# Kernel tuning notes

Hardware: AMD Instinct MI355X
Metric: run time of the kernel (lower is better)

The kernel has to match this reference:

```python
import jax, jax.numpy as jnp
import numpy as np

N, E, DIN, DH, H, B, C = 20000, 320000, 128, 64, 8, 16, 10
NEG_SLOPE = 0.2


def segment_softmax(e, dst, num_nodes):
    # e: [E, H] edge scores, softmax over edges sharing the same dst node
    m = jax.ops.segment_max(e, dst, num_segments=num_nodes)          # [N, H]
    ex = jnp.exp(e - m[dst])                                          # [E, H]
    den = jax.ops.segment_sum(ex, dst, num_segments=num_nodes)       # [N, H]
    return ex / den[dst]


def gat_layer(h, edge_src, edge_dst, W, attn_l, attn_r, bias):
    # h: [N, F_in] -> out: [N, H, DH]  (DGL GATConv math)
    feat = (h @ W).reshape(-1, H, DH)                                 # [N, H, DH]
    el = jnp.einsum('nhd,hd->nh', feat, attn_l)                       # [N, H]
    er = jnp.einsum('nhd,hd->nh', feat, attn_r)                       # [N, H]
    e = jax.nn.leaky_relu(el[edge_src] + er[edge_dst], NEG_SLOPE)     # [E, H]
    alpha = segment_softmax(e, edge_dst, feat.shape[0])               # [E, H]
    msg = feat[edge_src] * alpha[..., None]                           # [E, H, DH]
    out = jax.ops.segment_sum(msg, edge_dst, num_segments=feat.shape[0])
    return out + bias[None, :, :]


def setup_inputs() -> dict:
    key = jax.random.key(0)
    ks = jax.random.split(key, 16)
    s_in = 1.0 / np.sqrt(DIN)
    s_h = 1.0 / np.sqrt(DH)
    return {
        'g_feats': jax.random.normal(ks[0], (N, DIN), jnp.float32),
        'edge_src': jax.random.randint(ks[1], (E,), 0, N),
        'edge_dst': jax.random.randint(ks[2], (E,), 0, N),
        'node_graph_ids': jnp.sort(jax.random.randint(ks[3], (N,), 0, B)),
        'W_in': jax.random.normal(ks[4], (DIN, DH), jnp.float32) * s_in,
        'b_in': jnp.zeros((DH,), jnp.float32),
        'W1': jax.random.normal(ks[5], (DH, H * DH), jnp.float32) * s_h,
        'attn_l1': jax.random.normal(ks[6], (H, DH), jnp.float32) * s_h,
        'attn_r1': jax.random.normal(ks[7], (H, DH), jnp.float32) * s_h,
        'bias1': jnp.zeros((H, DH), jnp.float32),
        'W2': jax.random.normal(ks[8], (DH, H * DH), jnp.float32) * s_h,
        'attn_l2': jax.random.normal(ks[9], (H, DH), jnp.float32) * s_h,
        'attn_r2': jax.random.normal(ks[10], (H, DH), jnp.float32) * s_h,
        'bias2': jnp.zeros((H, DH), jnp.float32),
        'W_head': jax.random.normal(ks[11], (DH, C), jnp.float32) * s_h,
        'b_head': jnp.zeros((C,), jnp.float32),
    }


def reference(g_feats, edge_src, edge_dst, node_graph_ids,
              W_in, b_in, W1, attn_l1, attn_r1, bias1,
              W2, attn_l2, attn_r2, bias2, W_head, b_head):
    h = g_feats @ W_in + b_in                                          # input layer
    h = gat_layer(h, edge_src, edge_dst, W1, attn_l1, attn_r1, bias1)  # [N,H,DH]
    h = jax.nn.relu(h.mean(axis=1))                                    # head-mean + relu
    h = gat_layer(h, edge_src, edge_dst, W2, attn_l2, attn_r2, bias2)
    h = h.mean(axis=1)                                                 # [N, DH]
    # mean readout per graph
    sums = jax.ops.segment_sum(h, node_graph_ids, num_segments=B)      # [B, DH]
    cnt = jax.ops.segment_sum(jnp.ones((h.shape[0],), h.dtype), node_graph_ids, num_segments=B)
    hg = sums / jnp.maximum(cnt, 1.0)[:, None]
    return jax.nn.softmax(hg @ W_head + b_head, axis=-1)               # [B, C]
```

## Files before the change

kernel.cpp:

```cpp
#include <hip/hip_runtime.h>
#include <hip/hip_bf16.h>
#include <math.h>


#define NEG_SLOPE 0.2f

typedef float f32x2 __attribute__((ext_vector_type(2)));

__device__ __forceinline__ float bf2f(__hip_bfloat16 b) { return __bfloat162float(b); }

__device__ __forceinline__ unsigned int pack4_fp8(float a, float b, float c, float d) {
    unsigned int u = 0;
    u = __builtin_amdgcn_cvt_pk_fp8_f32(a, b, u, false);
    u = __builtin_amdgcn_cvt_pk_fp8_f32(c, d, u, true);
    return u;
}
__device__ __forceinline__ void unpack8_fp8(uint2 u, float* f) {
    f32x2 a = __builtin_amdgcn_cvt_pk_f32_fp8(u.x, false);
    f32x2 b = __builtin_amdgcn_cvt_pk_f32_fp8(u.x, true);
    f32x2 c = __builtin_amdgcn_cvt_pk_f32_fp8(u.y, false);
    f32x2 d = __builtin_amdgcn_cvt_pk_f32_fp8(u.y, true);
    f[0] = a[0]; f[1] = a[1]; f[2] = b[0]; f[3] = b[1];
    f[4] = c[0]; f[5] = c[1]; f[6] = d[0]; f[7] = d[1];
}

__global__ void hist_kernel(const int* __restrict__ dst, int* __restrict__ cnt, int E) {
    int e = blockIdx.x * 256 + threadIdx.x;
    if (e < E) atomicAdd(&cnt[dst[e]], 1);
}

__global__ __launch_bounds__(1024) void scan_kernel(const int* __restrict__ cnt,
                                                    int* __restrict__ row_start,
                                                    int* __restrict__ cursor, int N) {
    __shared__ int part[1024];
    int t = threadIdx.x;
    int CH = (N + 1023) >> 10;
    int beg = t * CH;
    int end = beg + CH; if (end > N) end = N;
    if (beg > N) beg = N;
    int local = 0;
    for (int i = beg; i < end; ++i) local += cnt[i];
    part[t] = local;
    __syncthreads();
    for (int off = 1; off < 1024; off <<= 1) {
        int v = (t >= off) ? part[t - off] : 0;
        __syncthreads();
        part[t] += v;
        __syncthreads();
    }
    int run = part[t] - local;
    for (int i = beg; i < end; ++i) {
        row_start[i] = run; cursor[i] = run;
        run += cnt[i];
    }
    if (t == 1023) row_start[N] = run;
}

__global__ void scatter_kernel(const int* __restrict__ src, const int* __restrict__ dst,
                               int* __restrict__ cursor, int* __restrict__ src_sorted, int E) {
    int e = blockIdx.x * 256 + threadIdx.x;
    if (e < E) {
        int p = atomicAdd(&cursor[dst[e]], 1);
        src_sorted[p] = src[e];
    }
}

__global__ __launch_bounds__(256) void in_gemm(const float* __restrict__ g,
                                               const float* __restrict__ W,
                                               const float* __restrict__ b,
                                               float* __restrict__ h0, int N) {
    __shared__ float gt[128][36];
    int t = threadIdx.x;
    int n0 = blockIdx.x * 32;
#pragma unroll
    for (int i = 0; i < 4; ++i) {
        int ch = t + i * 256;
        int r = ch >> 5, k0 = (ch & 31) << 2;
        float4 v = (n0 + r < N) ? *(const float4*)(g + (size_t)(n0 + r) * 128 + k0)
                                : make_float4(0.f, 0.f, 0.f, 0.f);
        gt[k0 + 0][r] = v.x; gt[k0 + 1][r] = v.y; gt[k0 + 2][r] = v.z; gt[k0 + 3][r] = v.w;
    }
    __syncthreads();
    int c = t & 63, rg = t >> 6;
    float acc[8];
#pragma unroll
    for (int j = 0; j < 8; ++j) acc[j] = 0.f;
#pragma unroll 4
    for (int k = 0; k < 128; ++k) {
        float w = W[k * 64 + c];
        const float* hp = &gt[k][rg * 8];
        float4 ha = *(const float4*)hp;
        float4 hb = *(const float4*)(hp + 4);
        acc[0] = fmaf(ha.x, w, acc[0]);
        acc[1] = fmaf(ha.y, w, acc[1]);
        acc[2] = fmaf(ha.z, w, acc[2]);
        acc[3] = fmaf(ha.w, w, acc[3]);
        acc[4] = fmaf(hb.x, w, acc[4]);
        acc[5] = fmaf(hb.y, w, acc[5]);
        acc[6] = fmaf(hb.z, w, acc[6]);
        acc[7] = fmaf(hb.w, w, acc[7]);
    }
    float bb = b[c];
#pragma unroll
    for (int j = 0; j < 8; ++j) {
        int r = rg * 8 + j;
        if (n0 + r < N) h0[(size_t)(n0 + r) * 64 + c] = acc[j] + bb;
    }
}

__global__ __launch_bounds__(512) void feat_gemm(const float* __restrict__ hin,
                                                 const float* __restrict__ W,
                                                 const float* __restrict__ al,
                                                 const float* __restrict__ ar,
                                                 unsigned char* __restrict__ feat8,
                                                 __hip_bfloat16* __restrict__ el,
                                                 __hip_bfloat16* __restrict__ er, int N) {
    __shared__ float ht[64][36];
    int t = threadIdx.x;
    int n0 = blockIdx.x * 32;
    {
        int r = t >> 4, k0 = (t & 15) << 2;
        float4 v = (n0 + r < N) ? *(const float4*)(hin + (size_t)(n0 + r) * 64 + k0)
                                : make_float4(0.f, 0.f, 0.f, 0.f);
        ht[k0 + 0][r] = v.x; ht[k0 + 1][r] = v.y; ht[k0 + 2][r] = v.z; ht[k0 + 3][r] = v.w;
    }
    __syncthreads();
    int ci = t & 127;
    int c0 = ci << 2;
    int rg = t >> 7;
    int r0 = rg << 3;
    float acc[8][4];
#pragma unroll
    for (int r = 0; r < 8; ++r)
#pragma unroll
        for (int j = 0; j < 4; ++j) acc[r][j] = 0.f;
#pragma unroll 4
    for (int k = 0; k < 64; ++k) {
        float4 w = *(const float4*)(W + k * 512 + c0);
        const float* hp = &ht[k][r0];
        float4 ha = *(const float4*)hp;
        float4 hb = *(const float4*)(hp + 4);
        float hr[8] = {ha.x, ha.y, ha.z, ha.w, hb.x, hb.y, hb.z, hb.w};
        float wv[4] = {w.x, w.y, w.z, w.w};
#pragma unroll
        for (int r = 0; r < 8; ++r)
#pragma unroll
            for (int j = 0; j < 4; ++j)
                acc[r][j] = fmaf(hr[r], wv[j], acc[r][j]);
    }
    float4 va = *(const float4*)(al + c0);
    float4 vb = *(const float4*)(ar + c0);
    int head = ci >> 4;
    float elp[8], erp[8];
#pragma unroll
    for (int r = 0; r < 8; ++r) {
        elp[r] = acc[r][0] * va.x + acc[r][1] * va.y + acc[r][2] * va.z + acc[r][3] * va.w;
        erp[r] = acc[r][0] * vb.x + acc[r][1] * vb.y + acc[r][2] * vb.z + acc[r][3] * vb.w;
        if (n0 + r0 + r < N) {
            *(unsigned int*)(feat8 + (size_t)(n0 + r0 + r) * 512 + c0) =
                pack4_fp8(acc[r][0], acc[r][1], acc[r][2], acc[r][3]);
        }
    }
#pragma unroll
    for (int off = 1; off < 16; off <<= 1)
#pragma unroll
        for (int r = 0; r < 8; ++r) {
            elp[r] += __shfl_xor(elp[r], off, 64);
            erp[r] += __shfl_xor(erp[r], off, 64);
        }
    if ((ci & 15) == 0) {
#pragma unroll
        for (int r = 0; r < 8; ++r) {
            if (n0 + r0 + r < N) {
                el[(size_t)(n0 + r0 + r) * 8 + head] = __float2bfloat16(elp[r]);
                er[(size_t)(n0 + r0 + r) * 8 + head] = __float2bfloat16(erp[r]);
            }
        }
    }
}

template <bool RELU>
__global__ __launch_bounds__(256) void gat_aggregate(
    const unsigned char* __restrict__ feat8, const __hip_bfloat16* __restrict__ el,
    const __hip_bfloat16* __restrict__ er, const float* __restrict__ bias,
    const int* __restrict__ row_start, const int* __restrict__ src_sorted,
    float* __restrict__ hout, int N) {
    int lane = threadIdx.x & 63;
    int n = blockIdx.x * 4 + (threadIdx.x >> 6);
    if (n >= N) return;
    int h = lane >> 3;
    float erh = bf2f(er[(size_t)n * 8 + h]);
    int row = row_start[n];
    int deg = row_start[n + 1] - row;
    const unsigned char* featl = feat8 + lane * 8;

    float acc[8];
#pragma unroll
    for (int j = 0; j < 8; ++j) acc[j] = 0.f;
    float den = 0.f;

    for (int base = 0; base < deg; base += 64) {
        int cnt = min(deg - base, 64);
        int sv = (lane < cnt) ? src_sorted[row + base + lane] : 0;
        int nsub = cnt & ~7;
        for (int i0 = 0; i0 < nsub; i0 += 8) {
            int se = __shfl(sv, i0 + (lane & 7), 64);
            float ve = bf2f(el[(size_t)se * 8 + h]) + erh;
            ve = fmaxf(ve, NEG_SLOPE * ve);
            float am = __expf(ve);
            int hb = lane & 0x38;
#pragma unroll
            for (int e = 0; e < 8; ++e) {
                float a = __shfl(am, hb | e, 64);
                int s = __shfl(sv, i0 + e, 64);
                uint2 u = *(const uint2*)(featl + (size_t)s * 512);
                den += a;
                float f[8];
                unpack8_fp8(u, f);
#pragma unroll
                for (int j = 0; j < 8; ++j) acc[j] = fmaf(a, f[j], acc[j]);
            }
        }
        for (int i = nsub; i < cnt; ++i) {
            int s = __shfl(sv, i, 64);
            uint2 u = *(const uint2*)(featl + (size_t)s * 512);
            float v = bf2f(el[(size_t)s * 8 + h]) + erh;
            v = fmaxf(v, NEG_SLOPE * v);
            float a = __expf(v);
            den += a;
            float f[8];
            unpack8_fp8(u, f);
#pragma unroll
            for (int j = 0; j < 8; ++j) acc[j] = fmaf(a, f[j], acc[j]);
        }
    }

    float invd = deg > 0 ? 1.f / den : 0.f;
    const float4* bp = (const float4*)(bias + lane * 8);
    float4 b0 = bp[0], b1 = bp[1];
    float o[8];
    o[0] = fmaf(acc[0], invd, b0.x); o[1] = fmaf(acc[1], invd, b0.y);
    o[2] = fmaf(acc[2], invd, b0.z); o[3] = fmaf(acc[3], invd, b0.w);
    o[4] = fmaf(acc[4], invd, b1.x); o[5] = fmaf(acc[5], invd, b1.y);
    o[6] = fmaf(acc[6], invd, b1.z); o[7] = fmaf(acc[7], invd, b1.w);

#pragma unroll
    for (int off = 8; off < 64; off <<= 1)
#pragma unroll
        for (int j = 0; j < 8; ++j)
            o[j] += __shfl_xor(o[j], off, 64);

    if (lane < 8) {
#pragma unroll
        for (int j = 0; j < 8; ++j) {
            o[j] *= 0.125f;
            if (RELU) o[j] = fmaxf(o[j], 0.f);
        }
        float4* op = (float4*)(hout + (size_t)n * 64 + lane * 8);
        op[0] = make_float4(o[0], o[1], o[2], o[3]);
        op[1] = make_float4(o[4], o[5], o[6], o[7]);
    }
}

__global__ __launch_bounds__(256) void readout_partial(const float* __restrict__ h2,
                                                       const int* __restrict__ gid,
                                                       float* __restrict__ hg, int N) {
    int c = threadIdx.x & 63;
    int r = threadIdx.x >> 6;
    int n0 = blockIdx.x * 256;
    float sum = 0.f; int cur = -1;
    int nend = n0 + 256; if (nend > N) nend = N;
    for (int n = n0 + r; n < nend; n += 4) {
        int g = gid[n];
        if (g != cur) {
            if (cur >= 0) atomicAdd(&hg[cur * 64 + c], sum);
            cur = g; sum = 0.f;
        }
        sum += h2[(size_t)n * 64 + c];
    }
    if (cur >= 0) atomicAdd(&hg[cur * 64 + c], sum);
}

__global__ __launch_bounds__(256) void head_kernel(const float* __restrict__ hg_sum,
                                                   const int* __restrict__ gid,
                                                   const float* __restrict__ W_head,
                                                   const float* __restrict__ b_head,
                                                   float* __restrict__ out, int N) {
    __shared__ int scnt[16];
    __shared__ float shg[16 * 64];
    __shared__ float slog[16 * 10];
    int t = threadIdx.x;
    if (t < 16) scnt[t] = 0;
    __syncthreads();
    for (int n = t; n < N; n += 256) atomicAdd(&scnt[gid[n]], 1);
    __syncthreads();
    for (int i = t; i < 1024; i += 256) {
        int g = i >> 6;
        shg[i] = hg_sum[i] / fmaxf((float)scnt[g], 1.f);
    }
    __syncthreads();
    if (t < 160) {
        int g = t / 10, c = t % 10;
        float acc = b_head[c];
#pragma unroll 16
        for (int k = 0; k < 64; ++k) acc = fmaf(shg[g * 64 + k], W_head[k * 10 + c], acc);
        slog[g * 10 + c] = acc;
    }
    __syncthreads();
    if (t < 16) {
        float mx = -INFINITY;
#pragma unroll
        for (int c = 0; c < 10; ++c) mx = fmaxf(mx, slog[t * 10 + c]);
        float e[10], s = 0.f;
#pragma unroll
        for (int c = 0; c < 10; ++c) { e[c] = __expf(slog[t * 10 + c] - mx); s += e[c]; }
        float inv = 1.f / s;
#pragma unroll
        for (int c = 0; c < 10; ++c) out[t * 10 + c] = e[c] * inv;
    }
}

extern "C" void kernel_launch(void* const* d_in, const int* in_sizes, int n_in,
                              void* d_out, int out_size, void* d_ws, size_t ws_size,
                              hipStream_t stream) {
    const float* g_feats  = (const float*)d_in[0];
    const int*   edge_src = (const int*)d_in[1];
    const int*   edge_dst = (const int*)d_in[2];
    const int*   gids     = (const int*)d_in[3];
    const float* W_in     = (const float*)d_in[4];
    const float* b_in     = (const float*)d_in[5];
    const float* W1       = (const float*)d_in[6];
    const float* attn_l1  = (const float*)d_in[7];
    const float* attn_r1  = (const float*)d_in[8];
    const float* bias1    = (const float*)d_in[9];
    const float* W2       = (const float*)d_in[10];
    const float* attn_l2  = (const float*)d_in[11];
    const float* attn_r2  = (const float*)d_in[12];
    const float* bias2    = (const float*)d_in[13];
    const float* W_head   = (const float*)d_in[14];
    const float* b_head   = (const float*)d_in[15];
    float* out = (float*)d_out;

    const int N = in_sizes[3];
    const int E = in_sizes[1];

    unsigned char* feat8 = (unsigned char*)d_ws;
    float* h0 = (float*)(feat8 + (size_t)N * 512);
    float* h1 = h0 + (size_t)N * 64;
    float* h2 = h1 + (size_t)N * 64;
    float* hg = h2 + (size_t)N * 64;
    __hip_bfloat16* el = (__hip_bfloat16*)(hg + 16 * 64);
    __hip_bfloat16* er = el + (size_t)N * 8;
    int* cnt        = (int*)(er + (size_t)N * 8);
    int* row_start  = cnt + N;
    int* cursor     = row_start + N + 1;
    int* src_sorted = cursor + N;

    hipMemsetAsync(cnt, 0, (size_t)N * 4, stream);
    hipMemsetAsync(hg, 0, 16 * 64 * 4, stream);

    int eb = (E + 255) / 256;
    int nb4 = (N + 3) / 4;
    int nb32 = (N + 31) / 32;
    int nb256 = (N + 255) / 256;

    hist_kernel<<<eb, 256, 0, stream>>>(edge_dst, cnt, E);
    scan_kernel<<<1, 1024, 0, stream>>>(cnt, row_start, cursor, N);
    scatter_kernel<<<eb, 256, 0, stream>>>(edge_src, edge_dst, cursor, src_sorted, E);

    in_gemm<<<nb32, 256, 0, stream>>>(g_feats, W_in, b_in, h0, N);

    feat_gemm<<<nb32, 512, 0, stream>>>(h0, W1, attn_l1, attn_r1, feat8, el, er, N);
    gat_aggregate<true><<<nb4, 256, 0, stream>>>(feat8, el, er, bias1, row_start, src_sorted, h1, N);

    feat_gemm<<<nb32, 512, 0, stream>>>(h1, W2, attn_l2, attn_r2, feat8, el, er, N);
    gat_aggregate<false><<<nb4, 256, 0, stream>>>(feat8, el, er, bias2, row_start, src_sorted, h2, N);

    readout_partial<<<nb256, 256, 0, stream>>>(h2, gids, hg, N);
    head_kernel<<<1, 256, 0, stream>>>(hg, gids, W_head, b_head, out, N);
}
```

Measured before the change: 321.9 us.

## Use bf16 MFMA for feature GEMM and batch attention exps in aggregation

```diff
diff --git a/kernel.cpp b/kernel.cpp
--- a/kernel.cpp
+++ b/kernel.cpp
@@ -6,14 +6,18 @@
 #define NEG_SLOPE 0.2f
 
 typedef float f32x2 __attribute__((ext_vector_type(2)));
+typedef float f32x4 __attribute__((ext_vector_type(4)));
+typedef short bf16x8 __attribute__((ext_vector_type(8)));
 
 __device__ __forceinline__ float bf2f(__hip_bfloat16 b) { return __bfloat162float(b); }
-
-__device__ __forceinline__ unsigned int pack4_fp8(float a, float b, float c, float d) {
-    unsigned int u = 0;
-    u = __builtin_amdgcn_cvt_pk_fp8_f32(a, b, u, false);
-    u = __builtin_amdgcn_cvt_pk_fp8_f32(c, d, u, true);
-    return u;
+__device__ __forceinline__ unsigned short f2bfu(float x) {
+    __hip_bfloat16 b = __float2bfloat16(x);
+    return *(unsigned short*)&b;
+}
+
+__device__ __forceinline__ unsigned char f2fp8(float x) {
+    unsigned int u = __builtin_amdgcn_cvt_pk_fp8_f32(x, x, 0, false);
+    return (unsigned char)(u & 0xff);
 }
 __device__ __forceinline__ void unpack8_fp8(uint2 u, float* f) {
     f32x2 a = __builtin_amdgcn_cvt_pk_f32_fp8(u.x, false);
@@ -63,6 +67,22 @@
         int p = atomicAdd(&cursor[dst[e]], 1);
         src_sorted[p] = src[e];
     }
+}
+
+__global__ __launch_bounds__(256) void wswiz_kernel(const float* __restrict__ W,
+                                                    unsigned short* __restrict__ Wswz) {
+    int fid = blockIdx.x * 256 + threadIdx.x;
+    int lane = fid & 63;
+    int ks = (fid >> 6) & 1;
+    int ctg = fid >> 7;
+    int col = ctg * 16 + (lane & 15);
+    int k0 = ks * 32 + ((lane >> 4) << 3);
+    unsigned short v[8];
+#pragma unroll
+    for (int j = 0; j < 8; ++j) v[j] = f2bfu(W[(k0 + j) * 512 + col]);
+    ushort4* dst = (ushort4*)(Wswz + (size_t)fid * 8);
+    dst[0] = make_ushort4(v[0], v[1], v[2], v[3]);
+    dst[1] = make_ushort4(v[4], v[5], v[6], v[7]);
 }
 
 __global__ __launch_bounds__(256) void in_gemm(const float* __restrict__ g,
@@ -109,72 +129,119 @@
 }
 
 __global__ __launch_bounds__(512) void feat_gemm(const float* __restrict__ hin,
-                                                 const float* __restrict__ W,
+                                                 const unsigned short* __restrict__ Wswz,
                                                  const float* __restrict__ al,
                                                  const float* __restrict__ ar,
                                                  unsigned char* __restrict__ feat8,
                                                  __hip_bfloat16* __restrict__ el,
                                                  __hip_bfloat16* __restrict__ er, int N) {
-    __shared__ float ht[64][36];
+    __shared__ unsigned short shA[32][72];
+    __shared__ unsigned char sfp8[32][512];
     int t = threadIdx.x;
     int n0 = blockIdx.x * 32;
     {
-        int r = t >> 4, k0 = (t & 15) << 2;
-        float4 v = (n0 + r < N) ? *(const float4*)(hin + (size_t)(n0 + r) * 64 + k0)
+        int r = t >> 4, c0 = (t & 15) << 2;
+        float4 v = (n0 + r < N) ? *(const float4*)(hin + (size_t)(n0 + r) * 64 + c0)
                                 : make_float4(0.f, 0.f, 0.f, 0.f);
-        ht[k0 + 0][r] = v.x; ht[k0 + 1][r] = v.y; ht[k0 + 2][r] = v.z; ht[k0 + 3][r] = v.w;
-    }
-    __syncthreads();
-    int ci = t & 127;
-    int c0 = ci << 2;
-    int rg = t >> 7;
-    int r0 = rg << 3;
-    float acc[8][4];
-#pragma unroll
-    for (int r = 0; r < 8; ++r)
-#pragma unroll
-        for (int j = 0; j < 4; ++j) acc[r][j] = 0.f;
-#pragma unroll 4
-    for (int k = 0; k < 64; ++k) {
-        float4 w = *(const float4*)(W + k * 512 + c0);
-        const float* hp = &ht[k][r0];
-        float4 ha = *(const float4*)hp;
-        float4 hb = *(const float4*)(hp + 4);
-        float hr[8] = {ha.x, ha.y, ha.z, ha.w, hb.x, hb.y, hb.z, hb.w};
-        float wv[4] = {w.x, w.y, w.z, w.w};
-#pragma unroll
-        for (int r = 0; r < 8; ++r)
+        *(ushort4*)&shA[r][c0] = make_ushort4(f2bfu(v.x), f2bfu(v.y), f2bfu(v.z), f2bfu(v.w));
+    }
+    __syncthreads();
+
+    int lane = t & 63;
+    int w = t >> 6;
+    int lr = lane & 15;
+    int lg = lane >> 4;
+
+    bf16x8 afrag[2][2];
+#pragma unroll
+    for (int rt = 0; rt < 2; ++rt)
+#pragma unroll
+        for (int ks = 0; ks < 2; ++ks)
+            afrag[rt][ks] = *(const bf16x8*)&shA[rt * 16 + lr][ks * 32 + lg * 8];
+
+    bf16x8 bfrag[4][2];
+#pragma unroll
+    for (int ct = 0; ct < 4; ++ct)
+#pragma unroll
+        for (int ks = 0; ks < 2; ++ks) {
+            int fid = ((w * 4 + ct) * 2 + ks) * 64 + lane;
+            bfrag[ct][ks] = *(const bf16x8*)(Wswz + (size_t)fid * 8);
+        }
+
+    f32x4 acc[2][4];
+#pragma unroll
+    for (int rt = 0; rt < 2; ++rt)
+#pragma unroll
+        for (int ct = 0; ct < 4; ++ct)
+            acc[rt][ct] = (f32x4){0.f, 0.f, 0.f, 0.f};
+
+#pragma unroll
+    for (int rt = 0; rt < 2; ++rt)
+#pragma unroll
+        for (int ct = 0; ct < 4; ++ct) {
+            acc[rt][ct] = __builtin_amdgcn_mfma_f32_16x16x32_bf16(afrag[rt][0], bfrag[ct][0], acc[rt][ct], 0, 0, 0);
+            acc[rt][ct] = __builtin_amdgcn_mfma_f32_16x16x32_bf16(afrag[rt][1], bfrag[ct][1], acc[rt][ct], 0, 0, 0);
+        }
+
+#pragma unroll
+    for (int rt = 0; rt < 2; ++rt)
+#pragma unroll
+        for (int ct = 0; ct < 4; ++ct) {
+            int col = w * 64 + ct * 16 + lr;
 #pragma unroll
             for (int j = 0; j < 4; ++j)
-                acc[r][j] = fmaf(hr[r], wv[j], acc[r][j]);
-    }
-    float4 va = *(const float4*)(al + c0);
-    float4 vb = *(const float4*)(ar + c0);
-    int head = ci >> 4;
-    float elp[8], erp[8];
-#pragma unroll
-    for (int r = 0; r < 8; ++r) {
-        elp[r] = acc[r][0] * va.x + acc[r][1] * va.y + acc[r][2] * va.z + acc[r][3] * va.w;
-        erp[r] = acc[r][0] * vb.x + acc[r][1] * vb.y + acc[r][2] * vb.z + acc[r][3] * vb.w;
-        if (n0 + r0 + r < N) {
-            *(unsigned int*)(feat8 + (size_t)(n0 + r0 + r) * 512 + c0) =
-                pack4_fp8(acc[r][0], acc[r][1], acc[r][2], acc[r][3]);
-        }
-    }
+                sfp8[rt * 16 + lg * 4 + j][col] = f2fp8(acc[rt][ct][j]);
+        }
+
+    float alv[4], arv[4];
+#pragma unroll
+    for (int ct = 0; ct < 4; ++ct) {
+        alv[ct] = al[w * 64 + ct * 16 + lr];
+        arv[ct] = ar[w * 64 + ct * 16 + lr];
+    }
+    float elp[2][4], erp[2][4];
+#pragma unroll
+    for (int rt = 0; rt < 2; ++rt)
+#pragma unroll
+        for (int j = 0; j < 4; ++j) {
+            float sl = 0.f, sr = 0.f;
+#pragma unroll
+            for (int ct = 0; ct < 4; ++ct) {
+                sl = fmaf(acc[rt][ct][j], alv[ct], sl);
+                sr = fmaf(acc[rt][ct][j], arv[ct], sr);
+            }
+            elp[rt][j] = sl; erp[rt][j] = sr;
+        }
 #pragma unroll
     for (int off = 1; off < 16; off <<= 1)
 #pragma unroll
-        for (int r = 0; r < 8; ++r) {
-            elp[r] += __shfl_xor(elp[r], off, 64);
-            erp[r] += __shfl_xor(erp[r], off, 64);
-        }
-    if ((ci & 15) == 0) {
-#pragma unroll
-        for (int r = 0; r < 8; ++r) {
-            if (n0 + r0 + r < N) {
-                el[(size_t)(n0 + r0 + r) * 8 + head] = __float2bfloat16(elp[r]);
-                er[(size_t)(n0 + r0 + r) * 8 + head] = __float2bfloat16(erp[r]);
+        for (int rt = 0; rt < 2; ++rt)
+#pragma unroll
+            for (int j = 0; j < 4; ++j) {
+                elp[rt][j] += __shfl_xor(elp[rt][j], off, 64);
+                erp[rt][j] += __shfl_xor(erp[rt][j], off, 64);
             }
+    if (lr == 0) {
+#pragma unroll
+        for (int rt = 0; rt < 2; ++rt)
+#pragma unroll
+            for (int j = 0; j < 4; ++j) {
+                int r = rt * 16 + lg * 4 + j;
+                if (n0 + r < N) {
+                    el[(size_t)(n0 + r) * 8 + w] = __float2bfloat16(elp[rt][j]);
+                    er[(size_t)(n0 + r) * 8 + w] = __float2bfloat16(erp[rt][j]);
+                }
+            }
+    }
+
+    __syncthreads();
+    {
+        const uint4* src = (const uint4*)&sfp8[0][0];
+        uint4* dst = (uint4*)(feat8 + (size_t)n0 * 512);
+        int i0 = t * 2;
+        if ((size_t)n0 * 512 + (size_t)(i0 + 2) * 16 <= (size_t)N * 512) {
+            dst[i0] = src[i0];
+            dst[i0 + 1] = src[i0 + 1];
         }
     }
 }
@@ -189,6 +256,8 @@
     int n = blockIdx.x * 4 + (threadIdx.x >> 6);
     if (n >= N) return;
     int h = lane >> 3;
+    int laneE = lane & 7;
+    int hb = lane & 0x38;
     float erh = bf2f(er[(size_t)n * 8 + h]);
     int row = row_start[n];
     int deg = row_start[n + 1] - row;
@@ -202,38 +271,57 @@
     for (int base = 0; base < deg; base += 64) {
         int cnt = min(deg - base, 64);
         int sv = (lane < cnt) ? src_sorted[row + base + lane] : 0;
-        int nsub = cnt & ~7;
-        for (int i0 = 0; i0 < nsub; i0 += 8) {
-            int se = __shfl(sv, i0 + (lane & 7), 64);
-            float ve = bf2f(el[(size_t)se * 8 + h]) + erh;
-            ve = fmaxf(ve, NEG_SLOPE * ve);
-            float am = __expf(ve);
-            int hb = lane & 0x38;
-#pragma unroll
-            for (int e = 0; e < 8; ++e) {
-                float a = __shfl(am, hb | e, 64);
-                int s = __shfl(sv, i0 + e, 64);
+
+        float am[8];
+#pragma unroll
+        for (int tt = 0; tt < 8; ++tt) {
+            if (tt * 8 < cnt) {
+                int idx = tt * 8 + laneE;
+                int se = __shfl(sv, idx, 64);
+                float ve = bf2f(el[(size_t)se * 8 + h]) + erh;
+                ve = fmaxf(ve, NEG_SLOPE * ve);
+                am[tt] = (idx < cnt) ? __expf(ve) : 0.f;
+            } else am[tt] = 0.f;
+        }
+#pragma unroll
+        for (int tt = 0; tt < 8; ++tt) den += am[tt];
+
+        int nfull = cnt >> 3;
+#pragma unroll
+        for (int tt = 0; tt < 8; ++tt) {
+            if (tt < nfull) {
+#pragma unroll
+                for (int e = 0; e < 8; ++e) {
+                    float a = __shfl(am[tt], hb | e, 64);
+                    int s = __shfl(sv, tt * 8 + e, 64);
+                    uint2 u = *(const uint2*)(featl + (size_t)s * 512);
+                    float f[8];
+                    unpack8_fp8(u, f);
+#pragma unroll
+                    for (int j = 0; j < 8; ++j) acc[j] = fmaf(a, f[j], acc[j]);
+                }
+            }
+        }
+        int ntl = nfull * 8;
+        if (ntl < cnt) {
+            float amt = 0.f;
+#pragma unroll
+            for (int tt = 0; tt < 8; ++tt)
+                if (tt == nfull) amt = am[tt];
+            for (int i = ntl; i < cnt; ++i) {
+                float a = __shfl(amt, hb | (i & 7), 64);
+                int s = __shfl(sv, i, 64);
                 uint2 u = *(const uint2*)(featl + (size_t)s * 512);
-                den += a;
                 float f[8];
                 unpack8_fp8(u, f);
 #pragma unroll
                 for (int j = 0; j < 8; ++j) acc[j] = fmaf(a, f[j], acc[j]);
             }
         }
-        for (int i = nsub; i < cnt; ++i) {
-            int s = __shfl(sv, i, 64);
-            uint2 u = *(const uint2*)(featl + (size_t)s * 512);
-            float v = bf2f(el[(size_t)s * 8 + h]) + erh;
-            v = fmaxf(v, NEG_SLOPE * v);
-            float a = __expf(v);
-            den += a;
-            float f[8];
-            unpack8_fp8(u, f);
-#pragma unroll
-            for (int j = 0; j < 8; ++j) acc[j] = fmaf(a, f[j], acc[j]);
-        }
-    }
+    }
+
+#pragma unroll
+    for (int off = 1; off < 8; off <<= 1) den += __shfl_xor(den, off, 64);
 
     float invd = deg > 0 ? 1.f / den : 0.f;
     const float4* bp = (const float4*)(bias + lane * 8);
@@ -351,7 +439,9 @@
     float* hg = h2 + (size_t)N * 64;
     __hip_bfloat16* el = (__hip_bfloat16*)(hg + 16 * 64);
     __hip_bfloat16* er = el + (size_t)N * 8;
-    int* cnt        = (int*)(er + (size_t)N * 8);
+    unsigned short* Wz1 = (unsigned short*)(er + (size_t)N * 8);
+    unsigned short* Wz2 = Wz1 + 32768;
+    int* cnt        = (int*)(Wz2 + 32768);
     int* row_start  = cnt + N;
     int* cursor     = row_start + N + 1;
     int* src_sorted = cursor + N;
@@ -368,12 +458,15 @@
     scan_kernel<<<1, 1024, 0, stream>>>(cnt, row_start, cursor, N);
     scatter_kernel<<<eb, 256, 0, stream>>>(edge_src, edge_dst, cursor, src_sorted, E);
 
+    wswiz_kernel<<<16, 256, 0, stream>>>(W1, Wz1);
+    wswiz_kernel<<<16, 256, 0, stream>>>(W2, Wz2);
+
     in_gemm<<<nb32, 256, 0, stream>>>(g_feats, W_in, b_in, h0, N);
 
-    feat_gemm<<<nb32, 512, 0, stream>>>(h0, W1, attn_l1, attn_r1, feat8, el, er, N);
+    feat_gemm<<<nb32, 512, 0, stream>>>(h0, Wz1, attn_l1, attn_r1, feat8, el, er, N);
     gat_aggregate<true><<<nb4, 256, 0, stream>>>(feat8, el, er, bias1, row_start, src_sorted, h1, N);
 
-    feat_gemm<<<nb32, 512, 0, stream>>>(h1, W2, attn_l2, attn_r2, feat8, el, er, N);
+    feat_gemm<<<nb32, 512, 0, stream>>>(h1, Wz2, attn_l2, attn_r2, feat8, el, er, N);
     gat_aggregate<false><<<nb4, 256, 0, stream>>>(feat8, el, er, bias2, row_start, src_sorted, h2, N);
 
     readout_partial<<<nb256, 256, 0, stream>>>(h2, gids, hg, N);
```

Measured after the change: 334.2 us. 1.04x slower.

## Reorder GAT layer to aggregate input features before projecting with MFMA GEMM

Applied to the files above, without the earlier changes.

```diff
diff --git a/kernel.cpp b/kernel.cpp
--- a/kernel.cpp
+++ b/kernel.cpp
@@ -5,23 +5,23 @@
 
 #define NEG_SLOPE 0.2f
 
-typedef float f32x2 __attribute__((ext_vector_type(2)));
+typedef float f32x4 __attribute__((ext_vector_type(4)));
+typedef short bf16x8 __attribute__((ext_vector_type(8)));
 
 __device__ __forceinline__ float bf2f(__hip_bfloat16 b) { return __bfloat162float(b); }
-
-__device__ __forceinline__ unsigned int pack4_fp8(float a, float b, float c, float d) {
-    unsigned int u = 0;
-    u = __builtin_amdgcn_cvt_pk_fp8_f32(a, b, u, false);
-    u = __builtin_amdgcn_cvt_pk_fp8_f32(c, d, u, true);
-    return u;
-}
-__device__ __forceinline__ void unpack8_fp8(uint2 u, float* f) {
-    f32x2 a = __builtin_amdgcn_cvt_pk_f32_fp8(u.x, false);
-    f32x2 b = __builtin_amdgcn_cvt_pk_f32_fp8(u.x, true);
-    f32x2 c = __builtin_amdgcn_cvt_pk_f32_fp8(u.y, false);
-    f32x2 d = __builtin_amdgcn_cvt_pk_f32_fp8(u.y, true);
-    f[0] = a[0]; f[1] = a[1]; f[2] = b[0]; f[3] = b[1];
-    f[4] = c[0]; f[5] = c[1]; f[6] = d[0]; f[7] = d[1];
+__device__ __forceinline__ unsigned short f2bfu(float x) {
+    __hip_bfloat16 b = __float2bfloat16(x);
+    return *(unsigned short*)&b;
+}
+__device__ __forceinline__ void unpack8_bf16(uint4 u, float* f) {
+    f[0] = __uint_as_float(u.x << 16);
+    f[1] = __uint_as_float(u.x & 0xffff0000u);
+    f[2] = __uint_as_float(u.y << 16);
+    f[3] = __uint_as_float(u.y & 0xffff0000u);
+    f[4] = __uint_as_float(u.z << 16);
+    f[5] = __uint_as_float(u.z & 0xffff0000u);
+    f[6] = __uint_as_float(u.w << 16);
+    f[7] = __uint_as_float(u.w & 0xffff0000u);
 }
 
 __global__ void hist_kernel(const int* __restrict__ dst, int* __restrict__ cnt, int E) {
@@ -65,11 +65,61 @@
     }
 }
 
+__global__ __launch_bounds__(256) void wprep_kernel(const float* __restrict__ W,
+                                                    const float* __restrict__ al,
+                                                    const float* __restrict__ ar,
+                                                    const float* __restrict__ bias,
+                                                    float* __restrict__ wl, float* __restrict__ wr,
+                                                    float* __restrict__ biasm) {
+    int t = threadIdx.x;
+    for (int i = t; i < 512; i += 256) {
+        int k = i >> 3, h = i & 7;
+        float sl = 0.f, sr = 0.f;
+#pragma unroll 8
+        for (int d = 0; d < 64; ++d) {
+            float wv = W[k * 512 + h * 64 + d];
+            sl = fmaf(wv, al[h * 64 + d], sl);
+            sr = fmaf(wv, ar[h * 64 + d], sr);
+        }
+        wl[i] = sl; wr[i] = sr;
+    }
+    if (t < 64) {
+        float s = 0.f;
+#pragma unroll
+        for (int h = 0; h < 8; ++h) s += bias[h * 64 + t];
+        biasm[t] = 0.125f * s;
+    }
+}
+
+__global__ __launch_bounds__(256) void wswizB_kernel(const float* __restrict__ W,
+                                                     unsigned short* __restrict__ Bz) {
+    int fid = blockIdx.x * 256 + threadIdx.x;
+    int lane = fid & 63;
+    int ks = (fid >> 6) & 15;
+    int ctg = fid >> 10;
+    int d = ctg * 16 + (lane & 15);
+    int K0 = ks * 32 + ((lane >> 4) << 3);
+    unsigned short v[8];
+#pragma unroll
+    for (int j = 0; j < 8; ++j) {
+        int K = K0 + j;
+        v[j] = f2bfu(W[(K & 63) * 512 + (K >> 6) * 64 + d]);
+    }
+    ushort4* dst = (ushort4*)(Bz + (size_t)fid * 8);
+    dst[0] = make_ushort4(v[0], v[1], v[2], v[3]);
+    dst[1] = make_ushort4(v[4], v[5], v[6], v[7]);
+}
+
 __global__ __launch_bounds__(256) void in_gemm(const float* __restrict__ g,
                                                const float* __restrict__ W,
                                                const float* __restrict__ b,
-                                               float* __restrict__ h0, int N) {
+                                               const float* __restrict__ wl,
+                                               const float* __restrict__ wr,
+                                               unsigned short* __restrict__ h0,
+                                               unsigned short* __restrict__ el,
+                                               unsigned short* __restrict__ er, int N) {
     __shared__ float gt[128][36];
+    __shared__ float sh[32][65];
     int t = threadIdx.x;
     int n0 = blockIdx.x * 32;
 #pragma unroll
@@ -104,95 +154,39 @@
 #pragma unroll
     for (int j = 0; j < 8; ++j) {
         int r = rg * 8 + j;
-        if (n0 + r < N) h0[(size_t)(n0 + r) * 64 + c] = acc[j] + bb;
-    }
-}
-
-__global__ __launch_bounds__(512) void feat_gemm(const float* __restrict__ hin,
-                                                 const float* __restrict__ W,
-                                                 const float* __restrict__ al,
-                                                 const float* __restrict__ ar,
-                                                 unsigned char* __restrict__ feat8,
-                                                 __hip_bfloat16* __restrict__ el,
-                                                 __hip_bfloat16* __restrict__ er, int N) {
-    __shared__ float ht[64][36];
-    int t = threadIdx.x;
-    int n0 = blockIdx.x * 32;
-    {
-        int r = t >> 4, k0 = (t & 15) << 2;
-        float4 v = (n0 + r < N) ? *(const float4*)(hin + (size_t)(n0 + r) * 64 + k0)
-                                : make_float4(0.f, 0.f, 0.f, 0.f);
-        ht[k0 + 0][r] = v.x; ht[k0 + 1][r] = v.y; ht[k0 + 2][r] = v.z; ht[k0 + 3][r] = v.w;
-    }
-    __syncthreads();
-    int ci = t & 127;
-    int c0 = ci << 2;
-    int rg = t >> 7;
-    int r0 = rg << 3;
-    float acc[8][4];
-#pragma unroll
-    for (int r = 0; r < 8; ++r)
-#pragma unroll
-        for (int j = 0; j < 4; ++j) acc[r][j] = 0.f;
-#pragma unroll 4
+        float v = acc[j] + bb;
+        sh[r][c] = v;
+        if (n0 + r < N) h0[(size_t)(n0 + r) * 64 + c] = f2bfu(v);
+    }
+    __syncthreads();
+    int r = t >> 3, hh = t & 7;
+    float sl = 0.f, sr = 0.f;
+#pragma unroll 8
     for (int k = 0; k < 64; ++k) {
-        float4 w = *(const float4*)(W + k * 512 + c0);
-        const float* hp = &ht[k][r0];
-        float4 ha = *(const float4*)hp;
-        float4 hb = *(const float4*)(hp + 4);
-        float hr[8] = {ha.x, ha.y, ha.z, ha.w, hb.x, hb.y, hb.z, hb.w};
-        float wv[4] = {w.x, w.y, w.z, w.w};
-#pragma unroll
-        for (int r = 0; r < 8; ++r)
-#pragma unroll
-            for (int j = 0; j < 4; ++j)
-                acc[r][j] = fmaf(hr[r], wv[j], acc[r][j]);
-    }
-    float4 va = *(const float4*)(al + c0);
-    float4 vb = *(const float4*)(ar + c0);
-    int head = ci >> 4;
-    float elp[8], erp[8];
-#pragma unroll
-    for (int r = 0; r < 8; ++r) {
-        elp[r] = acc[r][0] * va.x + acc[r][1] * va.y + acc[r][2] * va.z + acc[r][3] * va.w;
-        erp[r] = acc[r][0] * vb.x + acc[r][1] * vb.y + acc[r][2] * vb.z + acc[r][3] * vb.w;
-        if (n0 + r0 + r < N) {
-            *(unsigned int*)(feat8 + (size_t)(n0 + r0 + r) * 512 + c0) =
-                pack4_fp8(acc[r][0], acc[r][1], acc[r][2], acc[r][3]);
-        }
-    }
-#pragma unroll
-    for (int off = 1; off < 16; off <<= 1)
-#pragma unroll
-        for (int r = 0; r < 8; ++r) {
-            elp[r] += __shfl_xor(elp[r], off, 64);
-            erp[r] += __shfl_xor(erp[r], off, 64);
-        }
-    if ((ci & 15) == 0) {
-#pragma unroll
-        for (int r = 0; r < 8; ++r) {
-            if (n0 + r0 + r < N) {
-                el[(size_t)(n0 + r0 + r) * 8 + head] = __float2bfloat16(elp[r]);
-                er[(size_t)(n0 + r0 + r) * 8 + head] = __float2bfloat16(erp[r]);
-            }
-        }
-    }
-}
-
-template <bool RELU>
-__global__ __launch_bounds__(256) void gat_aggregate(
-    const unsigned char* __restrict__ feat8, const __hip_bfloat16* __restrict__ el,
-    const __hip_bfloat16* __restrict__ er, const float* __restrict__ bias,
+        float hv = sh[r][k];
+        sl = fmaf(hv, wl[k * 8 + hh], sl);
+        sr = fmaf(hv, wr[k * 8 + hh], sr);
+    }
+    if (n0 + r < N) {
+        el[(size_t)(n0 + r) * 8 + hh] = f2bfu(sl);
+        er[(size_t)(n0 + r) * 8 + hh] = f2bfu(sr);
+    }
+}
+
+__global__ __launch_bounds__(256, 8) void gat_h(
+    const unsigned short* __restrict__ hbf, const unsigned short* __restrict__ el,
+    const unsigned short* __restrict__ er,
     const int* __restrict__ row_start, const int* __restrict__ src_sorted,
-    float* __restrict__ hout, int N) {
+    unsigned short* __restrict__ aggn, int N) {
     int lane = threadIdx.x & 63;
     int n = blockIdx.x * 4 + (threadIdx.x >> 6);
     if (n >= N) return;
     int h = lane >> 3;
-    float erh = bf2f(er[(size_t)n * 8 + h]);
+    int dg = lane & 7;
+    float erh = bf2f(*(const __hip_bfloat16*)(er + (size_t)n * 8 + h));
     int row = row_start[n];
     int deg = row_start[n + 1] - row;
-    const unsigned char* featl = feat8 + lane * 8;
+    const unsigned short* hl = hbf + dg * 8;
 
     float acc[8];
 #pragma unroll
@@ -203,62 +197,131 @@
         int cnt = min(deg - base, 64);
         int sv = (lane < cnt) ? src_sorted[row + base + lane] : 0;
         int nsub = cnt & ~7;
+        int hb = lane & 0x38;
         for (int i0 = 0; i0 < nsub; i0 += 8) {
             int se = __shfl(sv, i0 + (lane & 7), 64);
-            float ve = bf2f(el[(size_t)se * 8 + h]) + erh;
+            float ve = bf2f(*(const __hip_bfloat16*)(el + (size_t)se * 8 + h)) + erh;
             ve = fmaxf(ve, NEG_SLOPE * ve);
             float am = __expf(ve);
-            int hb = lane & 0x38;
 #pragma unroll
             for (int e = 0; e < 8; ++e) {
                 float a = __shfl(am, hb | e, 64);
                 int s = __shfl(sv, i0 + e, 64);
-                uint2 u = *(const uint2*)(featl + (size_t)s * 512);
+                uint4 u = *(const uint4*)(hl + (size_t)s * 64);
                 den += a;
                 float f[8];
-                unpack8_fp8(u, f);
+                unpack8_bf16(u, f);
 #pragma unroll
                 for (int j = 0; j < 8; ++j) acc[j] = fmaf(a, f[j], acc[j]);
             }
         }
         for (int i = nsub; i < cnt; ++i) {
             int s = __shfl(sv, i, 64);
-            uint2 u = *(const uint2*)(featl + (size_t)s * 512);
-            float v = bf2f(el[(size_t)s * 8 + h]) + erh;
+            uint4 u = *(const uint4*)(hl + (size_t)s * 64);
+            float v = bf2f(*(const __hip_bfloat16*)(el + (size_t)s * 8 + h)) + erh;
             v = fmaxf(v, NEG_SLOPE * v);
             float a = __expf(v);
             den += a;
             float f[8];
-            unpack8_fp8(u, f);
+            unpack8_bf16(u, f);
 #pragma unroll
             for (int j = 0; j < 8; ++j) acc[j] = fmaf(a, f[j], acc[j]);
         }
     }
 
     float invd = deg > 0 ? 1.f / den : 0.f;
-    const float4* bp = (const float4*)(bias + lane * 8);
-    float4 b0 = bp[0], b1 = bp[1];
-    float o[8];
-    o[0] = fmaf(acc[0], invd, b0.x); o[1] = fmaf(acc[1], invd, b0.y);
-    o[2] = fmaf(acc[2], invd, b0.z); o[3] = fmaf(acc[3], invd, b0.w);
-    o[4] = fmaf(acc[4], invd, b1.x); o[5] = fmaf(acc[5], invd, b1.y);
-    o[6] = fmaf(acc[6], invd, b1.z); o[7] = fmaf(acc[7], invd, b1.w);
-
-#pragma unroll
-    for (int off = 8; off < 64; off <<= 1)
-#pragma unroll
-        for (int j = 0; j < 8; ++j)
-            o[j] += __shfl_xor(o[j], off, 64);
-
-    if (lane < 8) {
-#pragma unroll
-        for (int j = 0; j < 8; ++j) {
-            o[j] *= 0.125f;
-            if (RELU) o[j] = fmaxf(o[j], 0.f);
-        }
-        float4* op = (float4*)(hout + (size_t)n * 64 + lane * 8);
-        op[0] = make_float4(o[0], o[1], o[2], o[3]);
-        op[1] = make_float4(o[4], o[5], o[6], o[7]);
+    ushort4 s0 = make_ushort4(f2bfu(acc[0] * invd), f2bfu(acc[1] * invd),
+                              f2bfu(acc[2] * invd), f2bfu(acc[3] * invd));
+    ushort4 s1 = make_ushort4(f2bfu(acc[4] * invd), f2bfu(acc[5] * invd),
+                              f2bfu(acc[6] * invd), f2bfu(acc[7] * invd));
+    ushort4* op = (ushort4*)(aggn + (size_t)n * 512 + lane * 8);
+    op[0] = s0; op[1] = s1;
+}
+
+template <int LAYER>
+__global__ __launch_bounds__(256) void out_gemm(const unsigned short* __restrict__ aggn,
+                                                const unsigned short* __restrict__ Bz,
+                                                const float* __restrict__ biasm,
+                                                const float* __restrict__ wl,
+                                                const float* __restrict__ wr,
+                                                unsigned short* __restrict__ hnext_bf,
+                                                float* __restrict__ hnext_f,
+                                                unsigned short* __restrict__ el,
+                                                unsigned short* __restrict__ er, int N) {
+    __shared__ float sred[4][32][65];
+    int t = threadIdx.x;
+    int n0 = blockIdx.x * 32;
+    int lane = t & 63, w = t >> 6;
+    int lr = lane & 15, lg = lane >> 4;
+
+    f32x4 acc[2][4];
+#pragma unroll
+    for (int rt = 0; rt < 2; ++rt)
+#pragma unroll
+        for (int ct = 0; ct < 4; ++ct) acc[rt][ct] = (f32x4){0.f, 0.f, 0.f, 0.f};
+
+    int r0 = min(n0 + lr, N - 1);
+    int r1 = min(n0 + 16 + lr, N - 1);
+#pragma unroll
+    for (int ks2 = 0; ks2 < 4; ++ks2) {
+        int kofs = w * 128 + ks2 * 32 + lg * 8;
+        bf16x8 a0 = *(const bf16x8*)(aggn + (size_t)r0 * 512 + kofs);
+        bf16x8 a1 = *(const bf16x8*)(aggn + (size_t)r1 * 512 + kofs);
+#pragma unroll
+        for (int ct = 0; ct < 4; ++ct) {
+            int fid = (ct * 16 + (w * 4 + ks2)) * 64 + lane;
+            bf16x8 bf = *(const bf16x8*)(Bz + (size_t)fid * 8);
+            acc[0][ct] = __builtin_amdgcn_mfma_f32_16x16x32_bf16(a0, bf, acc[0][ct], 0, 0, 0);
+            acc[1][ct] = __builtin_amdgcn_mfma_f32_16x16x32_bf16(a1, bf, acc[1][ct], 0, 0, 0);
+        }
+    }
+#pragma unroll
+    for (int rt = 0; rt < 2; ++rt)
+#pragma unroll
+        for (int ct = 0; ct < 4; ++ct)
+#pragma unroll
+            for (int j = 0; j < 4; ++j)
+                sred[w][rt * 16 + lg * 4 + j][ct * 16 + lr] = acc[rt][ct][j];
+    __syncthreads();
+
+    int r = t >> 3, c0 = (t & 7) * 8;
+    float v[8];
+#pragma unroll
+    for (int j = 0; j < 8; ++j) {
+        int c = c0 + j;
+        float s = sred[0][r][c] + sred[1][r][c] + sred[2][r][c] + sred[3][r][c];
+        v[j] = s * 0.125f + biasm[c];
+        if (LAYER == 1) v[j] = fmaxf(v[j], 0.f);
+    }
+    if (LAYER == 1) {
+        if (n0 + r < N) {
+            ushort4 u0 = make_ushort4(f2bfu(v[0]), f2bfu(v[1]), f2bfu(v[2]), f2bfu(v[3]));
+            ushort4 u1 = make_ushort4(f2bfu(v[4]), f2bfu(v[5]), f2bfu(v[6]), f2bfu(v[7]));
+            ushort4* op = (ushort4*)(hnext_bf + (size_t)(n0 + r) * 64 + c0);
+            op[0] = u0; op[1] = u1;
+        }
+        __syncthreads();
+#pragma unroll
+        for (int j = 0; j < 8; ++j) sred[0][r][c0 + j] = v[j];
+        __syncthreads();
+        int hh = t & 7;
+        float sl = 0.f, sr = 0.f;
+#pragma unroll 8
+        for (int k = 0; k < 64; ++k) {
+            float hv = sred[0][r][k];
+            sl = fmaf(hv, wl[k * 8 + hh], sl);
+            sr = fmaf(hv, wr[k * 8 + hh], sr);
+        }
+        if (n0 + r < N) {
+            el[(size_t)(n0 + r) * 8 + hh] = f2bfu(sl);
+            er[(size_t)(n0 + r) * 8 + hh] = f2bfu(sr);
+        }
+    } else {
+        if (n0 + r < N) {
+            float4* op = (float4*)(hnext_f + (size_t)(n0 + r) * 64 + c0);
+            op[0] = make_float4(v[0], v[1], v[2], v[3]);
+            op[1] = make_float4(v[4], v[5], v[6], v[7]);
+        }
     }
 }
 
@@ -344,14 +407,22 @@
     const int N = in_sizes[3];
     const int E = in_sizes[1];
 
-    unsigned char* feat8 = (unsigned char*)d_ws;
-    float* h0 = (float*)(feat8 + (size_t)N * 512);
-    float* h1 = h0 + (size_t)N * 64;
-    float* h2 = h1 + (size_t)N * 64;
-    float* hg = h2 + (size_t)N * 64;
-    __hip_bfloat16* el = (__hip_bfloat16*)(hg + 16 * 64);
-    __hip_bfloat16* er = el + (size_t)N * 8;
-    int* cnt        = (int*)(er + (size_t)N * 8);
+    unsigned short* aggn = (unsigned short*)d_ws;
+    unsigned short* h0   = aggn + (size_t)N * 512;
+    unsigned short* h1   = h0 + (size_t)N * 64;
+    float* h2  = (float*)(h1 + (size_t)N * 64);
+    float* hg  = h2 + (size_t)N * 64;
+    unsigned short* el = (unsigned short*)(hg + 16 * 64);
+    unsigned short* er = el + (size_t)N * 8;
+    unsigned short* Bz1 = er + (size_t)N * 8;
+    unsigned short* Bz2 = Bz1 + 32768;
+    float* wl1 = (float*)(Bz2 + 32768);
+    float* wr1 = wl1 + 512;
+    float* wl2 = wr1 + 512;
+    float* wr2 = wl2 + 512;
+    float* biasm1 = wr2 + 512;
+    float* biasm2 = biasm1 + 64;
+    int* cnt        = (int*)(biasm2 + 64);
     int* row_start  = cnt + N;
     int* cursor     = row_start + N + 1;
     int* src_sorted = cursor + N;
@@ -368,13 +439,18 @@
     scan_kernel<<<1, 1024, 0, stream>>>(cnt, row_start, cursor, N);
     scatter_kernel<<<eb, 256, 0, stream>>>(edge_src, edge_dst, cursor, src_sorted, E);
 
-    in_gemm<<<nb32, 256, 0, stream>>>(g_feats, W_in, b_in, h0, N);
-
-    feat_gemm<<<nb32, 512, 0, stream>>>(h0, W1, attn_l1, attn_r1, feat8, el, er, N);
-    gat_aggregate<true><<<nb4, 256, 0, stream>>>(feat8, el, er, bias1, row_start, src_sorted, h1, N);
-
-    feat_gemm<<<nb32, 512, 0, stream>>>(h1, W2, attn_l2, attn_r2, feat8, el, er, N);
-    gat_aggregate<false><<<nb4, 256, 0, stream>>>(feat8, el, er, bias2, row_start, src_sorted, h2, N);
+    wprep_kernel<<<1, 256, 0, stream>>>(W1, attn_l1, attn_r1, bias1, wl1, wr1, biasm1);
+    wprep_kernel<<<1, 256, 0, stream>>>(W2, attn_l2, attn_r2, bias2, wl2, wr2, biasm2);
+    wswizB_kernel<<<16, 256, 0, stream>>>(W1, Bz1);
+    wswizB_kernel<<<16, 256, 0, stream>>>(W2, Bz2);
+
+    in_gemm<<<nb32, 256, 0, stream>>>(g_feats, W_in, b_in, wl1, wr1, h0, el, er, N);
+
+    gat_h<<<nb4, 256, 0, stream>>>(h0, el, er, row_start, src_sorted, aggn, N);
+    out_gemm<1><<<nb32, 256, 0, stream>>>(aggn, Bz1, biasm1, wl2, wr2, h1, nullptr, el, er, N);
+
+    gat_h<<<nb4, 256, 0, stream>>>(h1, el, er, row_start, src_sorted, aggn, N);
+    out_gemm<2><<<nb32, 256, 0, stream>>>(aggn, Bz2, biasm2, nullptr, nullptr, nullptr, h2, nullptr, nullptr, N);
 
     readout_partial<<<nb256, 256, 0, stream>>>(h2, gids, hg, N);
     head_kernel<<<1, 256, 0, stream>>>(hg, gids, W_head, b_head, out, N);
```

Result: faster. 311.8 us (-3.2%).
